# Kernel tuning notes

Hardware: AMD Instinct MI355X
Metric: run time of the kernel (lower is better)

## Reference

```python
import jax, jax.numpy as jnp
import numpy as np

EPS = 1e-6

def setup_inputs() -> dict:
    key = jax.random.key(0)
    kq, kk, kv = jax.random.split(key, 3)
    n, L, h, d = 4, 8192, 8, 64
    queries = jax.random.normal(kq, (n, L, h, d), dtype=jnp.float32)
    keys = jax.random.normal(kk, (n, L, h, d), dtype=jnp.float32)
    values = jax.random.normal(kv, (n, L, h, d), dtype=jnp.float32)
    return {"queries": queries, "keys": keys, "values": values}

def reference(queries, keys, values):
    d = queries.shape[-1]
    temp = d ** (-0.25)  # softmax_temp default e**-0.25
    # elu feature map: phi(x) = elu(x) + 1  (applied after temperature scaling)
    q = jax.nn.elu(queries * temp) + 1.0  # [n, l, h, d]
    k = jax.nn.elu(keys * temp) + 1.0     # [n, s, h, d]
    # associative kv state: [n, h, m, d]
    kv = jnp.einsum('nshd,nshm->nhmd', k, values)
    # normalizer z: [n, l, h]
    z = 1.0 / (jnp.einsum('nlhd,nhd->nlh', q, k.sum(axis=1)) + EPS)
    # output: [n, l, h, m]
    v = jnp.einsum('nlhd,nhmd,nlh->nlhm', q, kv, z)
    # module returns v.transpose(-3, -2) -> [n, h, l, m]
    return jnp.swapaxes(v, 1, 2)
```

## Files before the change

### kernel.cpp

```cpp
#include <hip/hip_runtime.h>
#include <hip/hip_bf16.h>

#define NN 4
#define LL 8192
#define HH 8
#define DD 64
#define NH 32
#define RS  (HH*DD)
#define KV_ELEMS 4160
#define CCH 128
#define TILE 16

typedef __attribute__((ext_vector_type(8))) short bf16x8;
typedef __attribute__((ext_vector_type(4))) float f32x4;

__device__ __forceinline__ float phi(float x) {
  float t = x * 0.35355339059327373f;
  return t > 0.f ? t + 1.f : __expf(t);
}
__device__ __forceinline__ short f2bf(float x) {
  __hip_bfloat16 h = __float2bfloat16(x);
  return (short)__builtin_bit_cast(unsigned short, h);
}
__device__ __forceinline__ float bf2f(short s) {
  __hip_bfloat16 h = __builtin_bit_cast(__hip_bfloat16, (unsigned short)s);
  return __bfloat162float(h);
}
__device__ __forceinline__ void split2(float x, short& hi, short& lo) {
  hi = f2bf(x);
  lo = f2bf(x - bf2f(hi));
}
#define MFMA16 __builtin_amdgcn_mfma_f32_16x16x32_bf16

__global__ __launch_bounds__(512, 1) void kv_partial_kernel(
    const float* __restrict__ K, const float* __restrict__ V,
    float* __restrict__ part, int sch)
{
  const int n = blockIdx.x / sch, chunk = blockIdx.x % sch;
  const int tid = threadIdx.x;
  const int h  = tid >> 6;
  const int t6 = tid & 63;
  const int d0 = ((t6 >> 3) & 7) * 8;
  const int m0 = (t6 & 7) * 8;
  const int hc = h * 64;
  const int sr = tid >> 5;
  const int sc = (tid & 31) * 16;
  const int rows_pb = LL / sch;
  const int nt = rows_pb / TILE;

  const float* kbase = K + ((size_t)n * LL + (size_t)chunk * rows_pb) * RS;
  const float* vbase = V + ((size_t)n * LL + (size_t)chunk * rows_pb) * RS;

  __shared__ float lds[2][2][TILE][520];

  float acc[8][8] = {};
  float ksacc[16] = {};
  f32x4 kr[4], vr[4];

  auto loadregs = [&](int T) {
    const float* kp = kbase + ((size_t)T * TILE + sr) * RS + sc;
    const float* vp = vbase + ((size_t)T * TILE + sr) * RS + sc;
#pragma unroll
    for (int i = 0; i < 4; ++i) {
      kr[i] = *(const f32x4*)(kp + 4 * i);
      vr[i] = *(const f32x4*)(vp + 4 * i);
    }
  };
  auto stage = [&](int b) {
#pragma unroll
    for (int i = 0; i < 4; ++i) {
      f32x4 kw;
#pragma unroll
      for (int j = 0; j < 4; ++j) {
        float f = phi(kr[i][j]);
        ksacc[4 * i + j] += f;
        kw[j] = f;
      }
      *(f32x4*)&lds[b][0][sr][sc + 4 * i] = kw;
      *(f32x4*)&lds[b][1][sr][sc + 4 * i] = vr[i];
    }
  };

  loadregs(0);
  stage(0);
  __syncthreads();

  for (int t = 0; t < nt; ++t) {
    const int cur = t & 1;
    if (t + 1 < nt) loadregs(t + 1);
#pragma unroll 2
    for (int s = 0; s < TILE; ++s) {
      const f32x4 k0 = *(const f32x4*)&lds[cur][0][s][hc + d0];
      const f32x4 k1 = *(const f32x4*)&lds[cur][0][s][hc + d0 + 4];
      const f32x4 v0 = *(const f32x4*)&lds[cur][1][s][hc + m0];
      const f32x4 v1 = *(const f32x4*)&lds[cur][1][s][hc + m0 + 4];
#pragma unroll
      for (int i = 0; i < 4; ++i)
#pragma unroll
        for (int j = 0; j < 4; ++j) {
          acc[i][j]         = fmaf(k0[i], v0[j], acc[i][j]);
          acc[i][j + 4]     = fmaf(k0[i], v1[j], acc[i][j + 4]);
          acc[i + 4][j]     = fmaf(k1[i], v0[j], acc[i + 4][j]);
          acc[i + 4][j + 4] = fmaf(k1[i], v1[j], acc[i + 4][j + 4]);
        }
    }
    if (t + 1 < nt) stage(cur ^ 1);
    __syncthreads();
  }

  float* po = part + ((size_t)blockIdx.x * 8 + h) * KV_ELEMS;
#pragma unroll
  for (int i = 0; i < 8; ++i) {
    f32x4 o0 = {acc[i][0], acc[i][1], acc[i][2], acc[i][3]};
    f32x4 o1 = {acc[i][4], acc[i][5], acc[i][6], acc[i][7]};
    *(f32x4*)&po[(d0 + i) * 64 + m0]     = o0;
    *(f32x4*)&po[(d0 + i) * 64 + m0 + 4] = o1;
  }

#pragma unroll
  for (int i = 0; i < 4; ++i) {
    f32x4 kw = {ksacc[4 * i], ksacc[4 * i + 1], ksacc[4 * i + 2], ksacc[4 * i + 3]};
    *(f32x4*)&lds[0][0][sr][sc + 4 * i] = kw;
  }
  __syncthreads();
  {
    float ssum = 0.f;
#pragma unroll
    for (int r = 0; r < TILE; ++r) ssum += lds[0][0][r][tid];
    part[((size_t)blockIdx.x * 8 + (tid >> 6)) * KV_ELEMS + 4096 + (tid & 63)] = ssum;
  }
}

__global__ __launch_bounds__(256) void kv_reduce_kernel(
    const float* __restrict__ part, short* __restrict__ kvh,
    short* __restrict__ kvl, float* __restrict__ ksum, int np)
{
  const int nh = blockIdx.x / 17;
  const int e  = (blockIdx.x % 17) * 256 + threadIdx.x;
  if (e >= KV_ELEMS) return;
  const int n = nh >> 3, hh = nh & 7;
  const float* pp = part + ((size_t)(n * np) * 8 + hh) * KV_ELEMS + e;
  float s = 0.f;
  for (int i = 0; i < np; ++i) s += pp[(size_t)i * 8 * KV_ELEMS];
  if (e < 4096) {
    const int d = e >> 6, m = e & 63;
    short hi, lo; split2(s, hi, lo);
    kvh[(size_t)nh * 4096 + m * 64 + d] = hi;
    kvl[(size_t)nh * 4096 + m * 64 + d] = lo;
  } else {
    ksum[(size_t)nh * 64 + (e - 4096)] = s;
  }
}

__global__ __launch_bounds__(512, 2) void attn_out_kernel(
    const float* __restrict__ Q, const short* __restrict__ kvh,
    const short* __restrict__ kvl, const float* __restrict__ ksumg,
    float* __restrict__ out)
{
  const int n = blockIdx.x / CCH, chunk = blockIdx.x % CCH;
  const int tid = threadIdx.x;
  const int w = tid >> 6, lane = tid & 63;
  const int q = lane >> 4, p = lane & 15;
  const int nh = n * 8 + w;
  const int rows_pb = LL / CCH;
  const int nt = rows_pb / 16;
  const int l_base = chunk * rows_pb;
  const int sr = tid >> 5, sc = (tid & 31) * 16;

  const float* qbase = Q + (size_t)n * LL * RS;

  __shared__ short qh[16][520];
  __shared__ short ql[16][520];

  bf16x8 bh[4][2], bl[4][2];
#pragma unroll
  for (int mt = 0; mt < 4; ++mt)
#pragma unroll
    for (int kst = 0; kst < 2; ++kst) {
      const size_t off = (size_t)nh * 4096 + (size_t)(mt * 16 + p) * 64 + kst * 32 + q * 8;
      bh[mt][kst] = *(const bf16x8*)(kvh + off);
      bl[mt][kst] = *(const bf16x8*)(kvl + off);
    }
  float ksr[2][8];
#pragma unroll
  for (int kst = 0; kst < 2; ++kst) {
    const float* kp = ksumg + (size_t)nh * 64 + kst * 32 + q * 8;
    f32x4 a = *(const f32x4*)(kp), b = *(const f32x4*)(kp + 4);
    ksr[kst][0]=a[0]; ksr[kst][1]=a[1]; ksr[kst][2]=a[2]; ksr[kst][3]=a[3];
    ksr[kst][4]=b[0]; ksr[kst][5]=b[1]; ksr[kst][6]=b[2]; ksr[kst][7]=b[3];
  }

  f32x4 qa[4], qb[4];
  auto loadq = [&](f32x4* R, int T) {
    const float* qp_ = qbase + (size_t)(l_base + T * 16 + sr) * RS + sc;
    R[0] = *(const f32x4*)(qp_);      R[1] = *(const f32x4*)(qp_ + 4);
    R[2] = *(const f32x4*)(qp_ + 8);  R[3] = *(const f32x4*)(qp_ + 12);
  };

  auto cbody = [&](const f32x4* R, int T) {
    bf16x8 hv0, hv1, lv0, lv1;
#pragma unroll
    for (int r = 0; r < 2; ++r)
#pragma unroll
      for (int jj = 0; jj < 4; ++jj) {
        float f = phi(R[r][jj]);
        short hs, ls; split2(f, hs, ls);
        hv0[r * 4 + jj] = hs; lv0[r * 4 + jj] = ls;
      }
#pragma unroll
    for (int r = 0; r < 2; ++r)
#pragma unroll
      for (int jj = 0; jj < 4; ++jj) {
        float f = phi(R[r + 2][jj]);
        short hs, ls; split2(f, hs, ls);
        hv1[r * 4 + jj] = hs; lv1[r * 4 + jj] = ls;
      }
    *(bf16x8*)&qh[sr][sc]     = hv0;  *(bf16x8*)&qh[sr][sc + 8] = hv1;
    *(bf16x8*)&ql[sr][sc]     = lv0;  *(bf16x8*)&ql[sr][sc + 8] = lv1;
    __syncthreads();

    f32x4 acc[4] = {};
    float zp = 0.f;
    bf16x8 ah[2], al[2];
#pragma unroll
    for (int kst = 0; kst < 2; ++kst) {
      const int cc = w * 64 + kst * 32 + q * 8;
      ah[kst] = *(const bf16x8*)&qh[p][cc];
      al[kst] = *(const bf16x8*)&ql[p][cc];
#pragma unroll
      for (int j = 0; j < 8; ++j)
        zp += (bf2f(ah[kst][j]) + bf2f(al[kst][j])) * ksr[kst][j];
    }
#pragma unroll
    for (int kst = 0; kst < 2; ++kst)
#pragma unroll
      for (int mt = 0; mt < 4; ++mt) {
        acc[mt] = MFMA16(ah[kst], bh[mt][kst], acc[mt], 0, 0, 0);
        acc[mt] = MFMA16(ah[kst], bl[mt][kst], acc[mt], 0, 0, 0);
        acc[mt] = MFMA16(al[kst], bh[mt][kst], acc[mt], 0, 0, 0);
      }
    zp += __shfl_xor(zp, 16, 64);
    zp += __shfl_xor(zp, 32, 64);
    const float z = 1.0f / (zp + 1e-6f);
    float zr[4];
#pragma unroll
    for (int r = 0; r < 4; ++r) zr[r] = __shfl(z, q * 4 + r, 64);

    const int l0 = l_base + T * 16;
#pragma unroll
    for (int mt = 0; mt < 4; ++mt)
#pragma unroll
      for (int r = 0; r < 4; ++r)
        out[((size_t)nh * LL + l0 + q * 4 + r) * DD + mt * 16 + p] = acc[mt][r] * zr[r];
    __syncthreads();
  };

  loadq(qa, 0);
  for (int t = 0; t < nt; t += 2) {
    loadq(qb, t + 1);
    cbody(qa, t);
    if (t + 2 < nt) loadq(qa, t + 2);
    cbody(qb, t + 1);
  }
}

extern "C" void kernel_launch(void* const* d_in, const int* in_sizes, int n_in,
                              void* d_out, int out_size, void* d_ws, size_t ws_size,
                              hipStream_t stream)
{
  const float* Q = (const float*)d_in[0];
  const float* K = (const float*)d_in[1];
  const float* V = (const float*)d_in[2];
  float* out = (float*)d_out;

  int sch = 64;
  while (sch > 4) {
    size_t need = (size_t)NN * sch * 8 * KV_ELEMS * 4
                + (size_t)NH * 4096 * 2 * 2
                + (size_t)NH * 64 * 4;
    if (need <= ws_size) break;
    sch >>= 1;
  }
  float* part = (float*)d_ws;
  short* kvh  = (short*)((char*)d_ws + (size_t)NN * sch * 8 * KV_ELEMS * 4);
  short* kvl  = kvh + (size_t)NH * 4096;
  float* ksum = (float*)(kvl + (size_t)NH * 4096);

  hipLaunchKernelGGL(kv_partial_kernel, dim3(NN * sch), dim3(512), 0, stream,
                     K, V, part, sch);
  hipLaunchKernelGGL(kv_reduce_kernel, dim3(NH * 17), dim3(256), 0, stream,
                     part, kvh, kvl, ksum, sch);
  hipLaunchKernelGGL(attn_out_kernel, dim3(NN * CCH), dim3(512), 0, stream,
                     Q, kvh, kvl, ksum, out);
}
```

Baseline: 247.1 us.

## Compute KV partial state with split-bf16 MFMA instead of scalar FP32 FMAs

The KV-state partial kernel moves from scalar FP32 outer-product FMAs to bf16 MFMA instructions. K features and V are split into hi/lo bf16 pairs and written transposed into swizzled LDS, and three MFMAs per tile keep precision close to FP32. The step size grows to 32 rows per iteration, with the global load for the next step issued after the barrier. The output kernel's trailing barrier also moves to just after the LDS reads, so the MFMA work and stores can overlap the next tile's staging. The hi/lo split adds conversion ALU work, and the LDS staging is no longer double-buffered.

```diff
diff --git a/kernel.cpp b/kernel.cpp
--- a/kernel.cpp
+++ b/kernel.cpp
@@ -9,7 +9,6 @@
 #define RS  (HH*DD)
 #define KV_ELEMS 4160
 #define CCH 128
-#define TILE 16
 
 typedef __attribute__((ext_vector_type(8))) short bf16x8;
 typedef __attribute__((ext_vector_type(4))) float f32x4;
@@ -38,96 +37,97 @@
 {
   const int n = blockIdx.x / sch, chunk = blockIdx.x % sch;
   const int tid = threadIdx.x;
-  const int h  = tid >> 6;
-  const int t6 = tid & 63;
-  const int d0 = ((t6 >> 3) & 7) * 8;
-  const int m0 = (t6 & 7) * 8;
-  const int hc = h * 64;
-  const int sr = tid >> 5;
-  const int sc = (tid & 31) * 16;
+  const int w = tid >> 6, lane = tid & 63;
+  const int q = lane >> 4, p = lane & 15;
+  const int cq = tid >> 7;
+  const int cg = tid & 127;
   const int rows_pb = LL / sch;
-  const int nt = rows_pb / TILE;
+  const int nsteps = rows_pb / 32;
 
   const float* kbase = K + ((size_t)n * LL + (size_t)chunk * rows_pb) * RS;
   const float* vbase = V + ((size_t)n * LL + (size_t)chunk * rows_pb) * RS;
 
-  __shared__ float lds[2][2][TILE][520];
-
-  float acc[8][8] = {};
-  float ksacc[16] = {};
-  f32x4 kr[4], vr[4];
+  __shared__ short pl[4][512 * 32];
+
+  f32x4 acc[4][4] = {};
+  float ksacc[4] = {0.f, 0.f, 0.f, 0.f};
+  f32x4 kr[8], vr[8];
 
   auto loadregs = [&](int T) {
-    const float* kp = kbase + ((size_t)T * TILE + sr) * RS + sc;
-    const float* vp = vbase + ((size_t)T * TILE + sr) * RS + sc;
-#pragma unroll
-    for (int i = 0; i < 4; ++i) {
-      kr[i] = *(const f32x4*)(kp + 4 * i);
-      vr[i] = *(const f32x4*)(vp + 4 * i);
-    }
-  };
-  auto stage = [&](int b) {
-#pragma unroll
-    for (int i = 0; i < 4; ++i) {
-      f32x4 kw;
-#pragma unroll
-      for (int j = 0; j < 4; ++j) {
-        float f = phi(kr[i][j]);
-        ksacc[4 * i + j] += f;
-        kw[j] = f;
-      }
-      *(f32x4*)&lds[b][0][sr][sc + 4 * i] = kw;
-      *(f32x4*)&lds[b][1][sr][sc + 4 * i] = vr[i];
+    const float* kp = kbase + (size_t)(T * 32 + cq * 8) * RS + 4 * cg;
+    const float* vp = vbase + (size_t)(T * 32 + cq * 8) * RS + 4 * cg;
+#pragma unroll
+    for (int u = 0; u < 8; ++u) {
+      kr[u] = *(const f32x4*)(kp + (size_t)u * RS);
+      vr[u] = *(const f32x4*)(vp + (size_t)u * RS);
+    }
+  };
+  auto cw = [&]() {
+#pragma unroll
+    for (int j = 0; j < 4; ++j) {
+      const int col = 4 * cg + j;
+      const int pos = (cq ^ ((col ^ (col >> 2)) & 3)) * 8;
+      bf16x8 kh, kl, vh, vl;
+      float s = 0.f;
+#pragma unroll
+      for (int u = 0; u < 8; ++u) {
+        float f = phi(kr[u][j]);
+        s += f;
+        short a, b;
+        split2(f, a, b);          kh[u] = a; kl[u] = b;
+        split2(vr[u][j], a, b);   vh[u] = a; vl[u] = b;
+      }
+      ksacc[j] += s;
+      *(bf16x8*)&pl[0][col * 32 + pos] = kh;
+      *(bf16x8*)&pl[1][col * 32 + pos] = kl;
+      *(bf16x8*)&pl[2][col * 32 + pos] = vh;
+      *(bf16x8*)&pl[3][col * 32 + pos] = vl;
     }
   };
 
   loadregs(0);
-  stage(0);
-  __syncthreads();
-
-  for (int t = 0; t < nt; ++t) {
-    const int cur = t & 1;
-    if (t + 1 < nt) loadregs(t + 1);
-#pragma unroll 2
-    for (int s = 0; s < TILE; ++s) {
-      const f32x4 k0 = *(const f32x4*)&lds[cur][0][s][hc + d0];
-      const f32x4 k1 = *(const f32x4*)&lds[cur][0][s][hc + d0 + 4];
-      const f32x4 v0 = *(const f32x4*)&lds[cur][1][s][hc + m0];
-      const f32x4 v1 = *(const f32x4*)&lds[cur][1][s][hc + m0 + 4];
-#pragma unroll
-      for (int i = 0; i < 4; ++i)
-#pragma unroll
-        for (int j = 0; j < 4; ++j) {
-          acc[i][j]         = fmaf(k0[i], v0[j], acc[i][j]);
-          acc[i][j + 4]     = fmaf(k0[i], v1[j], acc[i][j + 4]);
-          acc[i + 4][j]     = fmaf(k1[i], v0[j], acc[i + 4][j]);
-          acc[i + 4][j + 4] = fmaf(k1[i], v1[j], acc[i + 4][j + 4]);
-        }
-    }
-    if (t + 1 < nt) stage(cur ^ 1);
-    __syncthreads();
-  }
-
-  float* po = part + ((size_t)blockIdx.x * 8 + h) * KV_ELEMS;
-#pragma unroll
-  for (int i = 0; i < 8; ++i) {
-    f32x4 o0 = {acc[i][0], acc[i][1], acc[i][2], acc[i][3]};
-    f32x4 o1 = {acc[i][4], acc[i][5], acc[i][6], acc[i][7]};
-    *(f32x4*)&po[(d0 + i) * 64 + m0]     = o0;
-    *(f32x4*)&po[(d0 + i) * 64 + m0 + 4] = o1;
-  }
-
-#pragma unroll
-  for (int i = 0; i < 4; ++i) {
-    f32x4 kw = {ksacc[4 * i], ksacc[4 * i + 1], ksacc[4 * i + 2], ksacc[4 * i + 3]};
-    *(f32x4*)&lds[0][0][sr][sc + 4 * i] = kw;
-  }
+  for (int t = 0; t < nsteps; ++t) {
+    cw();
+    __syncthreads();
+    if (t + 1 < nsteps) loadregs(t + 1);
+
+    bf16x8 ah[4], al[4], bh[4], bl[4];
+#pragma unroll
+    for (int dt = 0; dt < 4; ++dt) {
+      const int col = w * 64 + dt * 16 + p;
+      const int pos = (q ^ ((col ^ (col >> 2)) & 3)) * 8;
+      ah[dt] = *(const bf16x8*)&pl[0][col * 32 + pos];
+      al[dt] = *(const bf16x8*)&pl[1][col * 32 + pos];
+      bh[dt] = *(const bf16x8*)&pl[2][col * 32 + pos];
+      bl[dt] = *(const bf16x8*)&pl[3][col * 32 + pos];
+    }
+#pragma unroll
+    for (int dt = 0; dt < 4; ++dt)
+#pragma unroll
+      for (int mt = 0; mt < 4; ++mt) {
+        acc[dt][mt] = MFMA16(ah[dt], bh[mt], acc[dt][mt], 0, 0, 0);
+        acc[dt][mt] = MFMA16(ah[dt], bl[mt], acc[dt][mt], 0, 0, 0);
+        acc[dt][mt] = MFMA16(al[dt], bh[mt], acc[dt][mt], 0, 0, 0);
+      }
+    __syncthreads();
+  }
+
+  float* po = part + ((size_t)blockIdx.x * 8 + w) * KV_ELEMS;
+#pragma unroll
+  for (int dt = 0; dt < 4; ++dt)
+#pragma unroll
+    for (int mt = 0; mt < 4; ++mt)
+#pragma unroll
+      for (int r = 0; r < 4; ++r)
+        po[(dt * 16 + q * 4 + r) * 64 + mt * 16 + p] = acc[dt][mt][r];
+
+  float* ksl = (float*)pl;
+  f32x4 kq = {ksacc[0], ksacc[1], ksacc[2], ksacc[3]};
+  *(f32x4*)&ksl[cq * 520 + 4 * cg] = kq;
   __syncthreads();
   {
-    float ssum = 0.f;
-#pragma unroll
-    for (int r = 0; r < TILE; ++r) ssum += lds[0][0][r][tid];
-    part[((size_t)blockIdx.x * 8 + (tid >> 6)) * KV_ELEMS + 4096 + (tid & 63)] = ssum;
+    float s = ksl[tid] + ksl[520 + tid] + ksl[1040 + tid] + ksl[1560 + tid];
+    part[((size_t)blockIdx.x * 8 + (tid >> 6)) * KV_ELEMS + 4096 + (tid & 63)] = s;
   }
 }
 
@@ -231,6 +231,8 @@
       for (int j = 0; j < 8; ++j)
         zp += (bf2f(ah[kst][j]) + bf2f(al[kst][j])) * ksr[kst][j];
     }
+    __syncthreads();
+
 #pragma unroll
     for (int kst = 0; kst < 2; ++kst)
 #pragma unroll
@@ -252,7 +254,6 @@
 #pragma unroll
       for (int r = 0; r < 4; ++r)
         out[((size_t)nh * LL + l0 + q * 4 + r) * DD + mt * 16 + p] = acc[mt][r] * zr[r];
-    __syncthreads();
   };
 
   loadq(qa, 0);
```

Result: no change. 245.7 us (-0.6%).
